# Kernel tuning notes

Hardware: AMD Instinct MI355X
Metric: run time of the kernel (lower is better)

The kernel has to match this reference:

```python
import jax, jax.numpy as jnp
import numpy as np

NEG_INF = -1000000000.0
B, N, D, H, L, DFF = 4, 1024, 512, 8, 6, 2048
DH = D // H
R2 = 10.0 ** 2  # locality_radius^2
EPS = 1e-5


def setup_inputs() -> dict:
    key = jax.random.key(0)
    ks = jax.random.split(key, 16)
    s = 0.02
    inp = {
        "tokens": jax.random.normal(ks[0], (B, N, D), jnp.float32),
        "xy": jax.random.uniform(ks[1], (B, N, 2), jnp.float32) * 100.0,
        "Wq": jax.random.normal(ks[2], (L, D, D), jnp.float32) * s,
        "Wk": jax.random.normal(ks[3], (L, D, D), jnp.float32) * s,
        "Wv": jax.random.normal(ks[4], (L, D, D), jnp.float32) * s,
        "Wo": jax.random.normal(ks[5], (L, D, D), jnp.float32) * s,
        "bo": jnp.zeros((L, D), jnp.float32),
        "W1": jax.random.normal(ks[6], (L, D, DFF), jnp.float32) * s,
        "b1": jnp.zeros((L, DFF), jnp.float32),
        "W2": jax.random.normal(ks[7], (L, DFF, D), jnp.float32) * s,
        "b2": jnp.zeros((L, D), jnp.float32),
        "g1": jnp.ones((L, D), jnp.float32),
        "be1": jnp.zeros((L, D), jnp.float32),
        "g2": jnp.ones((L, D), jnp.float32),
        "be2": jnp.zeros((L, D), jnp.float32),
        "gf": jnp.ones((D,), jnp.float32),
        "bf": jnp.zeros((D,), jnp.float32),
        "alive": jax.random.randint(ks[8], (B, N), 0, 2, dtype=jnp.int32),
        "species": jax.random.randint(ks[9], (B, N), 0, 3, dtype=jnp.int32),
        "n_agents": 512,
    }
    return inp


def _ln(x, g, b):
    m = jnp.mean(x, axis=-1, keepdims=True)
    v = jnp.mean((x - m) ** 2, axis=-1, keepdims=True)
    return (x - m) * jax.lax.rsqrt(v + EPS) * g + b


def _build_bias(alive, xy, species, dtype):
    # (B,1,N,N) additive bias, broadcast over heads (original repeats per head)
    af = alive.astype(dtype)
    bias = (1.0 - af)[:, None, None, :] * NEG_INF  # dead keys
    d2 = jnp.sum((xy[:, :, None, :] - xy[:, None, :, :]) ** 2, axis=-1)  # (B,N,N)
    bias = bias + jnp.where(d2 > R2, NEG_INF, 0.0)[:, None, :, :]
    ia = species < 2
    ip = species == 2
    ct = (ia[:, :, None] & ip[:, None, :]) | (ip[:, :, None] & ia[:, None, :])
    bias = bias + jnp.where(ct, NEG_INF, 0.0)[:, None, :, :]
    return bias


def reference(tokens, xy, Wq, Wk, Wv, Wo, bo, W1, b1, W2, b2,
              g1, be1, g2, be2, gf, bf, alive, species, n_agents):
    bias = _build_bias(alive, xy, species, tokens.dtype)
    scale = np.float32(np.sqrt(DH))
    x = tokens
    for l in range(L):
        h = _ln(x, g1[l], be1[l])
        q = (h @ Wq[l]).reshape(B, N, H, DH)
        k = (h @ Wk[l]).reshape(B, N, H, DH)
        v = (h @ Wv[l]).reshape(B, N, H, DH)
        scores = jnp.einsum('bihd,bjhd->bhij', q, k) / scale + bias
        w = jax.nn.softmax(scores, axis=-1)
        o = jnp.einsum('bhij,bjhd->bihd', w, v).reshape(B, N, D)
        x = x + (o @ Wo[l] + bo[l])
        h2 = _ln(x, g2[l], be2[l])
        ff = jax.nn.gelu(h2 @ W1[l] + b1[l], approximate=False) @ W2[l] + b2[l]
        x = x + ff
    return _ln(x, gf, bf)
```

## Files before the change

kernel.cpp:

```cpp
#include <hip/hip_runtime.h>
#include <math.h>

namespace {

constexpr int B = 4, N = 1024, D = 512, H = 8, DHd = 64, L = 6, DFFd = 2048;
constexpr int M = B * N;
constexpr int QKVS = 3 * D;
constexpr float NEG = -1000000000.0f;
constexpr float R2c = 100.0f;

typedef __attribute__((ext_vector_type(8))) short bf16x8;
typedef __attribute__((ext_vector_type(4))) float f32x4;

__device__ __forceinline__ short f2bf(float f) {
  union { float f; unsigned u; } c; c.f = f;
  unsigned r = (c.u + 0x7fffu + ((c.u >> 16) & 1u)) >> 16;
  return (short)r;
}

__device__ __forceinline__ float gelu_f(float x) {
  return 0.5f * x * (1.0f + erff(x * 0.70710678118654752f));
}

__global__ __launch_bounds__(256) void bias_kernel(
    const float* __restrict__ xy, const int* __restrict__ alive,
    const int* __restrict__ species, float* __restrict__ bias)
{
  int j = blockIdx.x * 256 + threadIdx.x;
  int i = blockIdx.y;
  int b = blockIdx.z;
  float xi = xy[((size_t)b * N + i) * 2 + 0];
  float yi = xy[((size_t)b * N + i) * 2 + 1];
  float xj = xy[((size_t)b * N + j) * 2 + 0];
  float yj = xy[((size_t)b * N + j) * 2 + 1];
  float dx = xi - xj, dy = yi - yj;
  float d2 = dx * dx + dy * dy;
  float bv = 0.0f;
  if (alive[b * N + j] == 0) bv += NEG;
  if (d2 > R2c) bv += NEG;
  int si = species[b * N + i], sj = species[b * N + j];
  bool ia = si < 2, ip = si == 2, ja = sj < 2, jp = sj == 2;
  if ((ia && jp) || (ip && ja)) bv += NEG;
  bias[((size_t)b * N + i) * N + j] = bv;
}

__global__ __launch_bounds__(256) void wprep_kernel(
    const float* __restrict__ src, short* __restrict__ dst,
    int K, int Nc, size_t srcLS, size_t dstLS)
{
  __shared__ float t[32][33];
  int k0 = blockIdx.x * 32, n0 = blockIdx.y * 32;
  src += (size_t)blockIdx.z * srcLS;
  dst += (size_t)blockIdx.z * dstLS;
  int r = threadIdx.x >> 5, c = threadIdx.x & 31;
#pragma unroll
  for (int i = 0; i < 4; ++i)
    t[r + i * 8][c] = src[(size_t)(k0 + r + i * 8) * Nc + n0 + c];
  __syncthreads();
#pragma unroll
  for (int i = 0; i < 4; ++i)
    dst[(size_t)(n0 + r + i * 8) * K + k0 + c] = f2bf(t[c][r + i * 8]);
}

__global__ __launch_bounds__(64) void ln_kernel(
    const float* __restrict__ x, const float* __restrict__ g,
    const float* __restrict__ be, float* __restrict__ outf,
    short* __restrict__ outb)
{
  int row = blockIdx.x;
  int tid = threadIdx.x;
  const float* xr = x + (size_t)row * D;
  float v[8];
  float sum = 0.f;
#pragma unroll
  for (int i = 0; i < 8; ++i) { v[i] = xr[tid + i * 64]; sum += v[i]; }
#pragma unroll
  for (int off = 32; off > 0; off >>= 1) sum += __shfl_down(sum, off);
  sum = __shfl(sum, 0);
  float mean = sum * (1.0f / D);
  float vs = 0.f;
#pragma unroll
  for (int i = 0; i < 8; ++i) { float d = v[i] - mean; vs += d * d; }
#pragma unroll
  for (int off = 32; off > 0; off >>= 1) vs += __shfl_down(vs, off);
  vs = __shfl(vs, 0);
  float rstd = rsqrtf(vs * (1.0f / D) + 1e-5f);
#pragma unroll
  for (int i = 0; i < 8; ++i) {
    int c = tid + i * 64;
    float o = (v[i] - mean) * rstd * g[c] + be[c];
    if (outb) outb[(size_t)row * D + c] = f2bf(o);
    else      outf[(size_t)row * D + c] = o;
  }
}

template <int BN, int NJ>
__global__ __launch_bounds__(256) void gemm_db_kernel(
    const short* __restrict__ A, const short* __restrict__ Bt,
    const float* __restrict__ bvec, float* __restrict__ Cf,
    short* __restrict__ Cb, int K, int Nc, int mode)
{
  __shared__ __align__(16) short As[2][128 * 32];
  __shared__ __align__(16) short Bs[2][BN * 32];
  const int bm = blockIdx.y * 128, bn = blockIdx.x * BN;
  const int t = threadIdx.x, wave = t >> 6, lane = t & 63;
  const int quad = lane >> 4, ln16 = lane & 15;
  const int wm = (wave & 1) * 64, wn = (wave >> 1) * (16 * NJ);
  const int srow = lane >> 2, sseg = lane & 3;
  constexpr int PEND = 2 + BN / 64;

  const short* Abase = A + (size_t)(bm + wave * 16 + srow) * K + sseg * 8;
  const short* Bbase = Bt + (size_t)(bn + wave * 16 + srow) * K + sseg * 8;
  const int nk = K >> 5;

  auto issue = [&](int p, int k0) {
#pragma unroll
    for (int h2 = 0; h2 < 2; ++h2) {
      __builtin_amdgcn_global_load_lds(
          (const __attribute__((address_space(1))) void*)(Abase + (size_t)h2 * 64 * K + k0),
          (__attribute__((address_space(3))) void*)&As[p][(wave * 16 + h2 * 64) * 32],
          16, 0, 0);
    }
#pragma unroll
    for (int h2 = 0; h2 < BN / 64; ++h2) {
      __builtin_amdgcn_global_load_lds(
          (const __attribute__((address_space(1))) void*)(Bbase + (size_t)h2 * 64 * K + k0),
          (__attribute__((address_space(3))) void*)&Bs[p][(wave * 16 + h2 * 64) * 32],
          16, 0, 0);
    }
  };

  f32x4 acc[4][NJ];
#pragma unroll
  for (int i = 0; i < 4; ++i)
#pragma unroll
    for (int j = 0; j < NJ; ++j) acc[i][j] = (f32x4){0.f, 0.f, 0.f, 0.f};

  issue(0, 0);
  for (int kt = 0; kt < nk; ++kt) {
    const int p = kt & 1;
    if (kt + 1 < nk) {
      issue(p ^ 1, (kt + 1) << 5);
      asm volatile("s_waitcnt vmcnt(%0)" :: "i"(PEND) : "memory");
    } else {
      asm volatile("s_waitcnt vmcnt(0)" ::: "memory");
    }
    asm volatile("s_barrier" ::: "memory");
    bf16x8 af[4], bfr[NJ];
#pragma unroll
    for (int i = 0; i < 4; ++i)
      af[i] = *(const bf16x8*)&As[p][(wm + i * 16 + ln16) * 32 + quad * 8];
#pragma unroll
    for (int j = 0; j < NJ; ++j)
      bfr[j] = *(const bf16x8*)&Bs[p][(wn + j * 16 + ln16) * 32 + quad * 8];
#pragma unroll
    for (int i = 0; i < 4; ++i)
#pragma unroll
      for (int j = 0; j < NJ; ++j)
        acc[i][j] = __builtin_amdgcn_mfma_f32_16x16x32_bf16(af[i], bfr[j], acc[i][j], 0, 0, 0);
    asm volatile("s_barrier" ::: "memory");
  }

  const int colbase = bn + wn + ln16;
#pragma unroll
  for (int i = 0; i < 4; ++i) {
#pragma unroll
    for (int r = 0; r < 4; ++r) {
      size_t row = (size_t)(bm + wm + i * 16 + quad * 4 + r);
      size_t off = row * Nc + colbase;
      if (mode == 0) {
#pragma unroll
        for (int j = 0; j < NJ; ++j) Cb[off + j * 16] = f2bf(acc[i][j][r]);
      } else if (mode == 1) {
#pragma unroll
        for (int j = 0; j < NJ; ++j) {
          float o = acc[i][j][r] + bvec[colbase + j * 16] + Cf[off + j * 16];
          Cf[off + j * 16] = o;
        }
      } else {
#pragma unroll
        for (int j = 0; j < NJ; ++j)
          Cb[off + j * 16] = f2bf(gelu_f(acc[i][j][r] + bvec[colbase + j * 16]));
      }
    }
  }
}

__global__ __launch_bounds__(256) void attn_mfma_kernel(
    const short* __restrict__ qkv, const float* __restrict__ bias,
    short* __restrict__ o)
{
  constexpr int LDR = 72;
  __shared__ __align__(16) short Qs[64 * LDR];
  __shared__ __align__(16) short Ks[64 * LDR];
  __shared__ __align__(16) short Vt[64 * LDR];
  __shared__ __align__(16) short Ps[4 * 16 * LDR];

  const int q0 = blockIdx.x * 64;
  const int hh = blockIdx.y;
  const int b  = blockIdx.z;
  const int t  = threadIdx.x;
  const int wave = t >> 6;
  const int lane = t & 63;
  const int quad = lane >> 4;
  const int ln16 = lane & 15;
  const int srow = t >> 2, sseg = t & 3;

  {
    const short* qb = qkv + (size_t)(b * N + q0 + srow) * QKVS + hh * 64 + sseg * 16;
    *(bf16x8*)&Qs[srow * LDR + sseg * 16] = *(const bf16x8*)qb;
    *(bf16x8*)&Qs[srow * LDR + sseg * 16 + 8] = *(const bf16x8*)(qb + 8);
  }

  float m_run[4], l_run[4];
  f32x4 Oacc[4];
#pragma unroll
  for (int r = 0; r < 4; ++r) { m_run[r] = -1e30f; l_run[r] = 0.f; }
#pragma unroll
  for (int dt = 0; dt < 4; ++dt) Oacc[dt] = (f32x4){0.f, 0.f, 0.f, 0.f};

  short* Psw = Ps + wave * 16 * LDR;
  const size_t brow0 = (size_t)(b * N + q0 + wave * 16 + quad * 4) * N;

  for (int kt = 0; kt < 16; ++kt) {
    const int k0 = kt * 64;
    __syncthreads();
    {
      const short* kb = qkv + (size_t)(b * N + k0 + srow) * QKVS + 512 + hh * 64 + sseg * 16;
      *(bf16x8*)&Ks[srow * LDR + sseg * 16] = *(const bf16x8*)kb;
      *(bf16x8*)&Ks[srow * LDR + sseg * 16 + 8] = *(const bf16x8*)(kb + 8);
      const short* vb = qkv + (size_t)(b * N + k0 + srow) * QKVS + 1024 + hh * 64 + sseg * 16;
      bf16x8 v0 = *(const bf16x8*)vb;
      bf16x8 v1 = *(const bf16x8*)(vb + 8);
#pragma unroll
      for (int e = 0; e < 8; ++e) {
        Vt[(sseg * 16 + e) * LDR + srow] = v0[e];
        Vt[(sseg * 16 + 8 + e) * LDR + srow] = v1[e];
      }
    }
    __syncthreads();

    bf16x8 a0 = *(const bf16x8*)&Qs[(wave * 16 + ln16) * LDR + quad * 8];
    bf16x8 a1 = *(const bf16x8*)&Qs[(wave * 16 + ln16) * LDR + 32 + quad * 8];
    f32x4 sc[4];
#pragma unroll
    for (int tile = 0; tile < 4; ++tile) {
      bf16x8 b0 = *(const bf16x8*)&Ks[(tile * 16 + ln16) * LDR + quad * 8];
      bf16x8 b1 = *(const bf16x8*)&Ks[(tile * 16 + ln16) * LDR + 32 + quad * 8];
      f32x4 z = (f32x4){0.f, 0.f, 0.f, 0.f};
      z = __builtin_amdgcn_mfma_f32_16x16x32_bf16(a0, b0, z, 0, 0, 0);
      z = __builtin_amdgcn_mfma_f32_16x16x32_bf16(a1, b1, z, 0, 0, 0);
      sc[tile] = z;
    }

    float s[4][4];
#pragma unroll
    for (int tile = 0; tile < 4; ++tile) {
      int col = k0 + tile * 16 + ln16;
#pragma unroll
      for (int r = 0; r < 4; ++r)
        s[tile][r] = sc[tile][r] * 0.125f + bias[brow0 + (size_t)r * N + col];
    }

    float p[4][4];
#pragma unroll
    for (int r = 0; r < 4; ++r) {
      float mt = fmaxf(fmaxf(s[0][r], s[1][r]), fmaxf(s[2][r], s[3][r]));
#pragma unroll
      for (int off = 1; off < 16; off <<= 1) mt = fmaxf(mt, __shfl_xor(mt, off));
      float m_new = fmaxf(m_run[r], mt);
      float al = __expf(m_run[r] - m_new);
      m_run[r] = m_new;
      float rs = 0.f;
#pragma unroll
      for (int tile = 0; tile < 4; ++tile) {
        float e = __expf(s[tile][r] - m_new);
        p[tile][r] = e;
        rs += e;
      }
#pragma unroll
      for (int off = 1; off < 16; off <<= 1) rs += __shfl_xor(rs, off);
      l_run[r] = l_run[r] * al + rs;
#pragma unroll
      for (int dt = 0; dt < 4; ++dt) Oacc[dt][r] *= al;
    }

#pragma unroll
    for (int tile = 0; tile < 4; ++tile)
#pragma unroll
      for (int r = 0; r < 4; ++r)
        Psw[(quad * 4 + r) * LDR + tile * 16 + ln16] = f2bf(p[tile][r]);
    __syncthreads();

    bf16x8 ap0 = *(const bf16x8*)&Psw[ln16 * LDR + quad * 8];
    bf16x8 ap1 = *(const bf16x8*)&Psw[ln16 * LDR + 32 + quad * 8];
#pragma unroll
    for (int dt = 0; dt < 4; ++dt) {
      bf16x8 bv0 = *(const bf16x8*)&Vt[(dt * 16 + ln16) * LDR + quad * 8];
      bf16x8 bv1 = *(const bf16x8*)&Vt[(dt * 16 + ln16) * LDR + 32 + quad * 8];
      Oacc[dt] = __builtin_amdgcn_mfma_f32_16x16x32_bf16(ap0, bv0, Oacc[dt], 0, 0, 0);
      Oacc[dt] = __builtin_amdgcn_mfma_f32_16x16x32_bf16(ap1, bv1, Oacc[dt], 0, 0, 0);
    }
  }

  float inv[4];
#pragma unroll
  for (int r = 0; r < 4; ++r) inv[r] = 1.0f / l_run[r];
#pragma unroll
  for (int dt = 0; dt < 4; ++dt) {
#pragma unroll
    for (int r = 0; r < 4; ++r) {
      int row = q0 + wave * 16 + quad * 4 + r;
      o[(size_t)(b * N + row) * D + hh * 64 + dt * 16 + ln16] =
          f2bf(Oacc[dt][r] * inv[r]);
    }
  }
}

}

extern "C" void kernel_launch(void* const* d_in, const int* in_sizes, int n_in,
                              void* d_out, int out_size, void* d_ws, size_t ws_size,
                              hipStream_t stream)
{
  const float* tokens  = (const float*)d_in[0];
  const float* xy      = (const float*)d_in[1];
  const float* Wq      = (const float*)d_in[2];
  const float* Wk      = (const float*)d_in[3];
  const float* Wv      = (const float*)d_in[4];
  const float* Wo      = (const float*)d_in[5];
  const float* bo      = (const float*)d_in[6];
  const float* W1      = (const float*)d_in[7];
  const float* b1      = (const float*)d_in[8];
  const float* W2      = (const float*)d_in[9];
  const float* b2      = (const float*)d_in[10];
  const float* g1      = (const float*)d_in[11];
  const float* be1     = (const float*)d_in[12];
  const float* g2      = (const float*)d_in[13];
  const float* be2     = (const float*)d_in[14];
  const float* gf      = (const float*)d_in[15];
  const float* bf      = (const float*)d_in[16];
  const int*   alive   = (const int*)d_in[17];
  const int*   species = (const int*)d_in[18];

  char* p = (char*)d_ws;
  float* bias = (float*)p; p += (size_t)B * N * N * 4;
  float* x    = (float*)p; p += (size_t)M * D * 4;
  short* h    = (short*)p; p += (size_t)M * D * 2;
  short* qkv  = (short*)p; p += (size_t)M * DFFd * 2;
  short* ff   = qkv;
  short* Wqkvt = (short*)p; p += (size_t)L * QKVS * D * 2;
  short* Wot   = (short*)p; p += (size_t)L * D * D * 2;
  short* W1t   = (short*)p; p += (size_t)L * DFFd * D * 2;
  short* W2t   = (short*)p; p += (size_t)L * D * DFFd * 2;

  hipMemcpyAsync(x, tokens, sizeof(float) * (size_t)M * D,
                 hipMemcpyDeviceToDevice, stream);
  bias_kernel<<<dim3(N / 256, N, B), 256, 0, stream>>>(xy, alive, species, bias);

  wprep_kernel<<<dim3(16, 16, L), 256, 0, stream>>>(
      Wq, Wqkvt + (size_t)0 * D * D, D, D, (size_t)D * D, (size_t)QKVS * D);
  wprep_kernel<<<dim3(16, 16, L), 256, 0, stream>>>(
      Wk, Wqkvt + (size_t)1 * D * D, D, D, (size_t)D * D, (size_t)QKVS * D);
  wprep_kernel<<<dim3(16, 16, L), 256, 0, stream>>>(
      Wv, Wqkvt + (size_t)2 * D * D, D, D, (size_t)D * D, (size_t)QKVS * D);
  wprep_kernel<<<dim3(16, 16, L), 256, 0, stream>>>(
      Wo, Wot, D, D, (size_t)D * D, (size_t)D * D);
  wprep_kernel<<<dim3(16, 64, L), 256, 0, stream>>>(
      W1, W1t, D, DFFd, (size_t)D * DFFd, (size_t)DFFd * D);
  wprep_kernel<<<dim3(64, 16, L), 256, 0, stream>>>(
      W2, W2t, DFFd, D, (size_t)DFFd * D, (size_t)D * DFFd);

  for (int l = 0; l < L; ++l) {
    ln_kernel<<<M, 64, 0, stream>>>(x, g1 + l * D, be1 + l * D, nullptr, h);
    gemm_db_kernel<128, 4><<<dim3(QKVS / 128, M / 128), 256, 0, stream>>>(
        h, Wqkvt + (size_t)l * QKVS * D, nullptr, nullptr, qkv, D, QKVS, 0);
    attn_mfma_kernel<<<dim3(N / 64, H, B), 256, 0, stream>>>(qkv, bias, h);
    gemm_db_kernel<64, 2><<<dim3(D / 64, M / 128), 256, 0, stream>>>(
        h, Wot + (size_t)l * D * D, bo + l * D, x, nullptr, D, D, 1);
    ln_kernel<<<M, 64, 0, stream>>>(x, g2 + l * D, be2 + l * D, nullptr, h);
    gemm_db_kernel<128, 4><<<dim3(DFFd / 128, M / 128), 256, 0, stream>>>(
        h, W1t + (size_t)l * DFFd * D, b1 + l * DFFd, nullptr, ff, D, DFFd, 2);
    gemm_db_kernel<64, 2><<<dim3(D / 64, M / 128), 256, 0, stream>>>(
        ff, W2t + (size_t)l * D * DFFd, b2 + l * D, x, nullptr, DFFd, D, 1);
  }
  ln_kernel<<<M, 64, 0, stream>>>(x, gf, bf, (float*)d_out, nullptr);
}
```

Baseline: 1.130 ms.

## Double-buffer K/V in attention, prefetch next tile, transpose score layout

The attention kernel now double-buffers K and V in shared memory and loads the next key tile and its bias values into registers while the current tile is being computed. That leaves one barrier per iteration instead of two. QK^T is computed as K·Q so each lane owns one query row, which turns the softmax max and sum reductions into two cross-quad shuffles and allows vectorized float4 bias loads. Risks are higher register and LDS use, and correctness depends on the hand-written lgkmcnt/barrier reasoning: the P write and read inside a wave happen with no block barrier, and the Ks/Vt buffer from two iterations back must not be overwritten too early.

New measurement: 1.038 ms. 1.09x faster.

```diff
diff --git a/kernel.cpp b/kernel.cpp
--- a/kernel.cpp
+++ b/kernel.cpp
@@ -192,8 +192,8 @@
 {
   constexpr int LDR = 72;
   __shared__ __align__(16) short Qs[64 * LDR];
-  __shared__ __align__(16) short Ks[64 * LDR];
-  __shared__ __align__(16) short Vt[64 * LDR];
+  __shared__ __align__(16) short Ks[2][64 * LDR];
+  __shared__ __align__(16) short Vt[2][64 * LDR];
   __shared__ __align__(16) short Ps[4 * 16 * LDR];
 
   const int q0 = blockIdx.x * 64;
@@ -211,108 +211,125 @@
     *(bf16x8*)&Qs[srow * LDR + sseg * 16] = *(const bf16x8*)qb;
     *(bf16x8*)&Qs[srow * LDR + sseg * 16 + 8] = *(const bf16x8*)(qb + 8);
   }
-
-  float m_run[4], l_run[4];
+  __syncthreads();
+
+  const int qrow = wave * 16 + ln16;
+  const bf16x8 qf0 = *(const bf16x8*)&Qs[qrow * LDR + quad * 8];
+  const bf16x8 qf1 = *(const bf16x8*)&Qs[qrow * LDR + 32 + quad * 8];
+
+  float m_run = -1e30f, l_run = 0.f;
   f32x4 Oacc[4];
 #pragma unroll
-  for (int r = 0; r < 4; ++r) { m_run[r] = -1e30f; l_run[r] = 0.f; }
-#pragma unroll
   for (int dt = 0; dt < 4; ++dt) Oacc[dt] = (f32x4){0.f, 0.f, 0.f, 0.f};
 
   short* Psw = Ps + wave * 16 * LDR;
-  const size_t brow0 = (size_t)(b * N + q0 + wave * 16 + quad * 4) * N;
+  const float* brow = bias + (size_t)(b * N + q0 + wave * 16 + ln16) * N;
+  const short* kb0 = qkv + (size_t)b * N * QKVS + 512 + hh * 64 + sseg * 16;
+  const short* vb0 = qkv + (size_t)b * N * QKVS + 1024 + hh * 64 + sseg * 16;
+
+  bf16x8 k0r = *(const bf16x8*)(kb0 + (size_t)srow * QKVS);
+  bf16x8 k1r = *(const bf16x8*)(kb0 + (size_t)srow * QKVS + 8);
+  bf16x8 v0r = *(const bf16x8*)(vb0 + (size_t)srow * QKVS);
+  bf16x8 v1r = *(const bf16x8*)(vb0 + (size_t)srow * QKVS + 8);
+  float4 b4[4];
+#pragma unroll
+  for (int ks = 0; ks < 4; ++ks)
+    b4[ks] = *(const float4*)&brow[ks * 16 + quad * 4];
 
   for (int kt = 0; kt < 16; ++kt) {
-    const int k0 = kt * 64;
-    __syncthreads();
-    {
-      const short* kb = qkv + (size_t)(b * N + k0 + srow) * QKVS + 512 + hh * 64 + sseg * 16;
-      *(bf16x8*)&Ks[srow * LDR + sseg * 16] = *(const bf16x8*)kb;
-      *(bf16x8*)&Ks[srow * LDR + sseg * 16 + 8] = *(const bf16x8*)(kb + 8);
-      const short* vb = qkv + (size_t)(b * N + k0 + srow) * QKVS + 1024 + hh * 64 + sseg * 16;
-      bf16x8 v0 = *(const bf16x8*)vb;
-      bf16x8 v1 = *(const bf16x8*)(vb + 8);
-#pragma unroll
-      for (int e = 0; e < 8; ++e) {
-        Vt[(sseg * 16 + e) * LDR + srow] = v0[e];
-        Vt[(sseg * 16 + 8 + e) * LDR + srow] = v1[e];
-      }
-    }
-    __syncthreads();
-
-    bf16x8 a0 = *(const bf16x8*)&Qs[(wave * 16 + ln16) * LDR + quad * 8];
-    bf16x8 a1 = *(const bf16x8*)&Qs[(wave * 16 + ln16) * LDR + 32 + quad * 8];
-    f32x4 sc[4];
-#pragma unroll
-    for (int tile = 0; tile < 4; ++tile) {
-      bf16x8 b0 = *(const bf16x8*)&Ks[(tile * 16 + ln16) * LDR + quad * 8];
-      bf16x8 b1 = *(const bf16x8*)&Ks[(tile * 16 + ln16) * LDR + 32 + quad * 8];
+    const int p = kt & 1;
+    *(bf16x8*)&Ks[p][srow * LDR + sseg * 16] = k0r;
+    *(bf16x8*)&Ks[p][srow * LDR + sseg * 16 + 8] = k1r;
+#pragma unroll
+    for (int e = 0; e < 8; ++e) {
+      Vt[p][(sseg * 16 + e) * LDR + srow] = v0r[e];
+      Vt[p][(sseg * 16 + 8 + e) * LDR + srow] = v1r[e];
+    }
+    const int k0n = (kt + 1 < 16) ? (kt + 1) * 64 : 0;
+    bf16x8 nk0 = *(const bf16x8*)(kb0 + (size_t)(k0n + srow) * QKVS);
+    bf16x8 nk1 = *(const bf16x8*)(kb0 + (size_t)(k0n + srow) * QKVS + 8);
+    bf16x8 nv0 = *(const bf16x8*)(vb0 + (size_t)(k0n + srow) * QKVS);
+    bf16x8 nv1 = *(const bf16x8*)(vb0 + (size_t)(k0n + srow) * QKVS + 8);
+    float4 bcur[4] = {b4[0], b4[1], b4[2], b4[3]};
+#pragma unroll
+    for (int ks = 0; ks < 4; ++ks)
+      b4[ks] = *(const float4*)&brow[k0n + ks * 16 + quad * 4];
+    asm volatile("s_waitcnt lgkmcnt(0)\n\ts_barrier" ::: "memory");
+
+    float sv[4][4];
+#pragma unroll
+    for (int ks = 0; ks < 4; ++ks) {
+      bf16x8 a0 = *(const bf16x8*)&Ks[p][(ks * 16 + ln16) * LDR + quad * 8];
+      bf16x8 a1 = *(const bf16x8*)&Ks[p][(ks * 16 + ln16) * LDR + 32 + quad * 8];
       f32x4 z = (f32x4){0.f, 0.f, 0.f, 0.f};
-      z = __builtin_amdgcn_mfma_f32_16x16x32_bf16(a0, b0, z, 0, 0, 0);
-      z = __builtin_amdgcn_mfma_f32_16x16x32_bf16(a1, b1, z, 0, 0, 0);
-      sc[tile] = z;
-    }
-
-    float s[4][4];
-#pragma unroll
-    for (int tile = 0; tile < 4; ++tile) {
-      int col = k0 + tile * 16 + ln16;
+      z = __builtin_amdgcn_mfma_f32_16x16x32_bf16(a0, qf0, z, 0, 0, 0);
+      z = __builtin_amdgcn_mfma_f32_16x16x32_bf16(a1, qf1, z, 0, 0, 0);
 #pragma unroll
       for (int r = 0; r < 4; ++r)
-        s[tile][r] = sc[tile][r] * 0.125f + bias[brow0 + (size_t)r * N + col];
-    }
-
-    float p[4][4];
-#pragma unroll
-    for (int r = 0; r < 4; ++r) {
-      float mt = fmaxf(fmaxf(s[0][r], s[1][r]), fmaxf(s[2][r], s[3][r]));
-#pragma unroll
-      for (int off = 1; off < 16; off <<= 1) mt = fmaxf(mt, __shfl_xor(mt, off));
-      float m_new = fmaxf(m_run[r], mt);
-      float al = __expf(m_run[r] - m_new);
-      m_run[r] = m_new;
-      float rs = 0.f;
-#pragma unroll
-      for (int tile = 0; tile < 4; ++tile) {
-        float e = __expf(s[tile][r] - m_new);
-        p[tile][r] = e;
+        sv[ks][r] = z[r] * 0.125f + (&bcur[ks].x)[r];
+    }
+
+    float mt = sv[0][0];
+#pragma unroll
+    for (int ks = 0; ks < 4; ++ks)
+#pragma unroll
+      for (int r = 0; r < 4; ++r) mt = fmaxf(mt, sv[ks][r]);
+    mt = fmaxf(mt, __shfl_xor(mt, 16));
+    mt = fmaxf(mt, __shfl_xor(mt, 32));
+    const float m_new = fmaxf(m_run, mt);
+    const float alpha = __expf(m_run - m_new);
+    m_run = m_new;
+    float rs = 0.f;
+    float pv[4][4];
+#pragma unroll
+    for (int ks = 0; ks < 4; ++ks)
+#pragma unroll
+      for (int r = 0; r < 4; ++r) {
+        float e = __expf(sv[ks][r] - m_new);
+        pv[ks][r] = e;
         rs += e;
       }
-#pragma unroll
-      for (int off = 1; off < 16; off <<= 1) rs += __shfl_xor(rs, off);
-      l_run[r] = l_run[r] * al + rs;
-#pragma unroll
-      for (int dt = 0; dt < 4; ++dt) Oacc[dt][r] *= al;
-    }
-
-#pragma unroll
-    for (int tile = 0; tile < 4; ++tile)
-#pragma unroll
-      for (int r = 0; r < 4; ++r)
-        Psw[(quad * 4 + r) * LDR + tile * 16 + ln16] = f2bf(p[tile][r]);
-    __syncthreads();
+    rs += __shfl_xor(rs, 16);
+    rs += __shfl_xor(rs, 32);
+    l_run = l_run * alpha + rs;
+    float af[4];
+#pragma unroll
+    for (int r = 0; r < 4; ++r) af[r] = __shfl(alpha, quad * 4 + r);
+#pragma unroll
+    for (int dt = 0; dt < 4; ++dt)
+#pragma unroll
+      for (int r = 0; r < 4; ++r) Oacc[dt][r] *= af[r];
+
+#pragma unroll
+    for (int ks = 0; ks < 4; ++ks) {
+      short4 pk = {f2bf(pv[ks][0]), f2bf(pv[ks][1]), f2bf(pv[ks][2]), f2bf(pv[ks][3])};
+      *(short4*)&Psw[ln16 * LDR + ks * 16 + quad * 4] = pk;
+    }
 
     bf16x8 ap0 = *(const bf16x8*)&Psw[ln16 * LDR + quad * 8];
     bf16x8 ap1 = *(const bf16x8*)&Psw[ln16 * LDR + 32 + quad * 8];
 #pragma unroll
     for (int dt = 0; dt < 4; ++dt) {
-      bf16x8 bv0 = *(const bf16x8*)&Vt[(dt * 16 + ln16) * LDR + quad * 8];
-      bf16x8 bv1 = *(const bf16x8*)&Vt[(dt * 16 + ln16) * LDR + 32 + quad * 8];
+      bf16x8 bv0 = *(const bf16x8*)&Vt[p][(dt * 16 + ln16) * LDR + quad * 8];
+      bf16x8 bv1 = *(const bf16x8*)&Vt[p][(dt * 16 + ln16) * LDR + 32 + quad * 8];
       Oacc[dt] = __builtin_amdgcn_mfma_f32_16x16x32_bf16(ap0, bv0, Oacc[dt], 0, 0, 0);
       Oacc[dt] = __builtin_amdgcn_mfma_f32_16x16x32_bf16(ap1, bv1, Oacc[dt], 0, 0, 0);
     }
-  }
-
-  float inv[4];
-#pragma unroll
-  for (int r = 0; r < 4; ++r) inv[r] = 1.0f / l_run[r];
+
+    k0r = nk0; k1r = nk1; v0r = nv0; v1r = nv1;
+  }
+
+  const float linv = 1.0f / l_run;
+  float iv[4];
+#pragma unroll
+  for (int r = 0; r < 4; ++r) iv[r] = __shfl(linv, quad * 4 + r);
 #pragma unroll
   for (int dt = 0; dt < 4; ++dt) {
 #pragma unroll
     for (int r = 0; r < 4; ++r) {
       int row = q0 + wave * 16 + quad * 4 + r;
       o[(size_t)(b * N + row) * D + hh * 64 + dt * 16 + ln16] =
-          f2bf(Oacc[dt][r] * inv[r]);
+          f2bf(Oacc[dt][r] * iv[r]);
     }
   }
 }
```
